# Kernel optimization log

Measured on AMD Instinct MI355X. Metric: run time of the kernel, lower is better.

## Reference

```python
import jax, jax.numpy as jnp
import numpy as np

MAX_DEPTH = 12  # 2^12-1 = 4095 internal nodes, 4096 leaves
NUM_INPUT = 1024
NUM_OUTPUT = 1024
BATCH = 4096


def setup_inputs() -> dict:
    key = jax.random.key(0)
    k1, k2, k3 = jax.random.split(key, 3)
    n_internal = (1 << MAX_DEPTH) - 1
    n_leaves = 1 << MAX_DEPTH
    x = jax.random.normal(k1, (BATCH, NUM_INPUT), dtype=jnp.float32)
    # per-node weights ~ N(0, 0.1) as in nn.Parameter(torch.empty(num_input).normal_(0, 0.1))
    W = jax.random.normal(k2, (n_internal, NUM_INPUT), dtype=jnp.float32) * 0.1
    b = jnp.zeros((n_internal,), dtype=jnp.float32)
    # leaf prob_dist initialized to ones in the original
    leaf = jnp.ones((n_leaves, NUM_OUTPUT), dtype=jnp.float32)
    # use random leaves so the blend is non-trivial for correctness checking
    leaf = leaf + jax.random.normal(k3, (n_leaves, NUM_OUTPUT), dtype=jnp.float32)
    return {"x": x, "W": W, "b": b, "leaf": leaf}


def reference(x, W, b, leaf):
    # W rows are internal nodes in level order: [root | level1 (2) | level2 (4) | ...]
    # Gate value at each node: sigmoid(x . w + b); output blends right with weight g,
    # left with weight (1-g), recursively -> leaf mixture weights are products of
    # gate / (1-gate) along each root-to-leaf path.
    B = x.shape[0]
    g = jax.nn.sigmoid(jnp.einsum('bi,ni->bn', x, W) + b)  # [B, n_internal]
    probs = jnp.ones((B, 1), dtype=x.dtype)
    idx = 0
    for d in range(MAX_DEPTH):  # structural loop over tree levels (fixed, small)
        n = 1 << d
        gl = g[:, idx:idx + n]  # gates at level d, [B, n]
        idx += n
        # children interleaved: [L0, R0, L1, R1, ...]; left weight (1-g), right g
        probs = jnp.stack([probs * (1.0 - gl), probs * gl], axis=-1).reshape(B, 2 * n)
    # output = sum over leaves of path_prob * leaf_dist
    out = jnp.einsum('bl,lo->bo', probs, leaf)  # [B, num_output]
    return out
```

## Files before the change

### kernel.cpp

```cpp
#include <hip/hip_runtime.h>
#include <hip/hip_bf16.h>
#include <hip/hip_fp16.h>

typedef _Float16 half8 __attribute__((ext_vector_type(8)));
typedef _Float16 half4 __attribute__((ext_vector_type(4)));
typedef float floatx4 __attribute__((ext_vector_type(4)));

#define BATCH   4096
#define NIN     1024
#define NODES   4095
#define NPAD    4096
#define NOUT    1024
#define NLEAF   4096
#define SPLITK  4

__device__ __forceinline__ void gload_lds16(const void* g, void* l) {
    __builtin_amdgcn_global_load_lds(
        (const __attribute__((address_space(1))) void*)g,
        (__attribute__((address_space(3))) void*)l, 16, 0, 0);
}

#define BAR() asm volatile("s_barrier" ::: "memory")

__global__ void k_f32_to_f16_pad(const float* __restrict__ src,
                                 _Float16* __restrict__ dst, int n, int nsrc) {
    int i = (blockIdx.x * blockDim.x + threadIdx.x) * 4;
    if (i >= n) return;
    float4 v;
    if (i < nsrc) v = *(const float4*)(src + i);
    else          v = make_float4(0.f, 0.f, 0.f, 0.f);
    half4 h;
    h.x = (_Float16)v.x; h.y = (_Float16)v.y;
    h.z = (_Float16)v.z; h.w = (_Float16)v.w;
    *(half4*)(dst + i) = h;
}

__global__ void k_transpose_f16(const float* __restrict__ src,
                                _Float16* __restrict__ dst) {
    __shared__ _Float16 t[32][33];
    int l0 = blockIdx.x * 32, o0 = blockIdx.y * 32;
    int tx = threadIdx.x & 31, ty = threadIdx.x >> 5;
#pragma unroll
    for (int i = 0; i < 4; i++) {
        int l = l0 + ty + i * 8;
        t[ty + i * 8][tx] = (_Float16)src[(size_t)l * NOUT + o0 + tx];
    }
    __syncthreads();
#pragma unroll
    for (int i = 0; i < 4; i++) {
        int o = o0 + ty + i * 8;
        dst[(size_t)o * NLEAF + l0 + tx] = t[tx][ty + i * 8];
    }
}

#define MFMA_CL(QR, QC, BARR, KK)                                               \
  _Pragma("unroll") for (int fr = 0; fr < 4; fr++)                              \
    _Pragma("unroll") for (int fc = 0; fc < 2; fc++)                            \
      acc[QR][QC][fr][fc] = __builtin_amdgcn_mfma_f32_16x16x32_f16(             \
          af[fr][KK], BARR[fc][KK], acc[QR][QC][fr][fc], 0, 0, 0);

template <int EPILOGUE>
__launch_bounds__(512, 2)
__global__ void gemm256(const _Float16* __restrict__ A,
                        const _Float16* __restrict__ Bm,
                        const float* __restrict__ bias,
                        void* __restrict__ C,
                        int M, int N, int K, int ldc, int Klen) {
    __shared__ __align__(16) _Float16 As[2][2][128 * 64];
    __shared__ __align__(16) _Float16 Bs[2][2][128 * 64];
    const int tid  = threadIdx.x;
    const int lane = tid & 63;
    const int wid  = tid >> 6;
    const int wm   = wid >> 2;
    const int wn   = wid & 3;
    const int m0 = blockIdx.y * 256;
    const int n0 = blockIdx.x * 256;
    const int k0 = blockIdx.z * Klen;
    (void)N;

    floatx4 acc[2][2][4][2] = {};
    half8 af[4][2];
    half8 bf0[2][2];
    half8 bf1[2][2];

    const int r1 = tid >> 3;
    const int c1 = (tid & 7) ^ (r1 & 7);
    const _Float16* Abase = A  + (size_t)(m0 + r1) * K + k0 + c1 * 8;
    const _Float16* Bbase = Bm + (size_t)(n0 + r1) * K + k0 + c1 * 8;

    auto stageA = [&](int bufx, int h, int T) {
        const _Float16* s = Abase + (size_t)h * 128 * K + T * 64;
        gload_lds16(s,                    &As[bufx][h][tid * 8]);
        gload_lds16(s + (size_t)64 * K,   &As[bufx][h][4096 + tid * 8]);
    };
    auto stageB = [&](int bufx, int h, int T) {
        const _Float16* s = Bbase + (size_t)h * 128 * K + T * 64;
        gload_lds16(s,                    &Bs[bufx][h][tid * 8]);
        gload_lds16(s + (size_t)64 * K,   &Bs[bufx][h][4096 + tid * 8]);
    };

    const int l4   = lane >> 4;
    const int arow = wm * 64 + (lane & 15);
    const int brow = wn * 32 + (lane & 15);
    const int pA0 = ((l4)     ^ (arow & 7)) * 8;
    const int pA1 = ((4 + l4) ^ (arow & 7)) * 8;
    const int pB0 = ((l4)     ^ (brow & 7)) * 8;
    const int pB1 = ((4 + l4) ^ (brow & 7)) * 8;

    const int NTt = Klen >> 6;

    stageA(0, 0, 0); stageB(0, 0, 0); stageA(0, 1, 0); stageB(0, 1, 0);
    if (NTt > 1) {
        stageA(1, 0, 1); stageB(1, 1, 1);
        asm volatile("s_waitcnt vmcnt(4)" ::: "memory");
    } else {
        asm volatile("s_waitcnt vmcnt(0)" ::: "memory");
    }
    BAR();

    for (int T = 0; T < NTt; ++T) {
        const int buf = T & 1;
        const _Float16* A0 = &As[buf][0][0];
        const _Float16* A1 = &As[buf][1][0];
        const _Float16* B0 = &Bs[buf][0][0];
        const _Float16* B1 = &Bs[buf][1][0];

#pragma unroll
        for (int fr = 0; fr < 4; fr++) {
            af[fr][0] = *(const half8*)(A0 + (arow + fr * 16) * 64 + pA0);
            af[fr][1] = *(const half8*)(A0 + (arow + fr * 16) * 64 + pA1);
        }
#pragma unroll
        for (int fc = 0; fc < 2; fc++) {
            bf0[fc][0] = *(const half8*)(B0 + (brow + fc * 16) * 64 + pB0);
            bf0[fc][1] = *(const half8*)(B0 + (brow + fc * 16) * 64 + pB1);
        }
        if (T + 1 < NTt) stageA(buf ^ 1, 1, T + 1);
        __builtin_amdgcn_s_setprio(1);
        MFMA_CL(0, 0, bf0, 0);
        MFMA_CL(0, 0, bf0, 1);
        __builtin_amdgcn_s_setprio(0);
        BAR();

#pragma unroll
        for (int fc = 0; fc < 2; fc++) {
            bf1[fc][0] = *(const half8*)(B1 + (brow + fc * 16) * 64 + pB0);
            bf1[fc][1] = *(const half8*)(B1 + (brow + fc * 16) * 64 + pB1);
        }
        if (T + 1 < NTt) stageB(buf ^ 1, 0, T + 1);
        __builtin_amdgcn_s_setprio(1);
        MFMA_CL(0, 1, bf1, 0);
        MFMA_CL(0, 1, bf1, 1);
        __builtin_amdgcn_s_setprio(0);
        BAR();

#pragma unroll
        for (int fr = 0; fr < 4; fr++) {
            af[fr][0] = *(const half8*)(A1 + (arow + fr * 16) * 64 + pA0);
            af[fr][1] = *(const half8*)(A1 + (arow + fr * 16) * 64 + pA1);
        }
        if (T + 2 < NTt) stageA(buf, 0, T + 2);
        __builtin_amdgcn_s_setprio(1);
        MFMA_CL(1, 1, bf1, 0);
        MFMA_CL(1, 1, bf1, 1);
        __builtin_amdgcn_s_setprio(0);
        BAR();

        if (T + 2 < NTt) stageB(buf, 1, T + 2);
        __builtin_amdgcn_s_setprio(1);
        MFMA_CL(1, 0, bf0, 0);
        MFMA_CL(1, 0, bf0, 1);
        __builtin_amdgcn_s_setprio(0);
        if (T + 1 < NTt) {
            if (T + 2 < NTt) asm volatile("s_waitcnt vmcnt(4)" ::: "memory");
            else             asm volatile("s_waitcnt vmcnt(0)" ::: "memory");
        }
        BAR();
    }

    const int erow = m0 + wm * 64 + l4 * 4;
    const int ecol = n0 + wn * 32 + (lane & 15);
    _Float16* Cp = (_Float16*)C + (EPILOGUE == 2 ? (size_t)blockIdx.z * M * ldc : 0);
#pragma unroll
    for (int qr = 0; qr < 2; qr++)
#pragma unroll
        for (int qc = 0; qc < 2; qc++)
#pragma unroll
            for (int fr = 0; fr < 4; fr++)
#pragma unroll
                for (int fc = 0; fc < 2; fc++) {
                    const int col = ecol + qc * 128 + fc * 16;
#pragma unroll
                    for (int rj = 0; rj < 4; rj++) {
                        const int row = erow + qr * 128 + fr * 16 + rj;
                        float v = acc[qr][qc][fr][fc][rj];
                        if (EPILOGUE == 1) {
                            float bb = (col < NODES) ? bias[col] : 0.f;
                            float z = v + bb;
                            Cp[(size_t)row * ldc + col] =
                                (_Float16)(1.f / (1.f + __expf(-z)));
                        } else {
                            Cp[(size_t)row * ldc + col] = (_Float16)v;
                        }
                    }
                }
}

__global__ void k_reduce4(const _Float16* __restrict__ part, float* __restrict__ out) {
    const size_t S = (size_t)BATCH * NOUT;
    size_t i = ((size_t)blockIdx.x * 256 + threadIdx.x) * 8;
    half8 a = *(const half8*)(part + i);
    half8 b = *(const half8*)(part + S + i);
    half8 c = *(const half8*)(part + 2 * S + i);
    half8 d = *(const half8*)(part + 3 * S + i);
    float4 lo, hi;
    lo.x = (float)a[0] + (float)b[0] + (float)c[0] + (float)d[0];
    lo.y = (float)a[1] + (float)b[1] + (float)c[1] + (float)d[1];
    lo.z = (float)a[2] + (float)b[2] + (float)c[2] + (float)d[2];
    lo.w = (float)a[3] + (float)b[3] + (float)c[3] + (float)d[3];
    hi.x = (float)a[4] + (float)b[4] + (float)c[4] + (float)d[4];
    hi.y = (float)a[5] + (float)b[5] + (float)c[5] + (float)d[5];
    hi.z = (float)a[6] + (float)b[6] + (float)c[6] + (float)d[6];
    hi.w = (float)a[7] + (float)b[7] + (float)c[7] + (float)d[7];
    *(float4*)(out + i) = lo;
    *(float4*)(out + i + 4) = hi;
}

__global__ void k_probs(const _Float16* __restrict__ g,
                        _Float16* __restrict__ probs) {
    __shared__ float gs[NPAD];
    const int b = blockIdx.x;
    const _Float16* grow = g + (size_t)b * NPAD;
#pragma unroll
    for (int it = 0; it < 2; it++) {
        int i = threadIdx.x + it * 256;
        half8 v = *(const half8*)(grow + i * 8);
#pragma unroll
        for (int j = 0; j < 8; j++) gs[i * 8 + j] = (float)v[j];
    }
    __syncthreads();
    const int t = threadIdx.x;
    float p = 1.f;
#pragma unroll
    for (int d = 0; d < 8; d++) {
        int node = (1 << d) - 1 + (t >> (8 - d));
        float gg = gs[node];
        int bit = (t >> (7 - d)) & 1;
        p *= bit ? gg : (1.f - gg);
    }
    float p9[2], p10[4], p11[8], p12[16];
    {
        float gg = gs[255 + t];
        p9[0] = p * (1.f - gg); p9[1] = p * gg;
    }
#pragma unroll
    for (int i = 0; i < 2; i++) {
        float gg = gs[511 + 2 * t + i];
        p10[2 * i] = p9[i] * (1.f - gg); p10[2 * i + 1] = p9[i] * gg;
    }
#pragma unroll
    for (int i = 0; i < 4; i++) {
        float gg = gs[1023 + 4 * t + i];
        p11[2 * i] = p10[i] * (1.f - gg); p11[2 * i + 1] = p10[i] * gg;
    }
#pragma unroll
    for (int i = 0; i < 8; i++) {
        float gg = gs[2047 + 8 * t + i];
        p12[2 * i] = p11[i] * (1.f - gg); p12[2 * i + 1] = p11[i] * gg;
    }
    half8 o0, o1;
#pragma unroll
    for (int j = 0; j < 8; j++) { o0[j] = (_Float16)p12[j]; o1[j] = (_Float16)p12[8 + j]; }
    _Float16* pr = probs + (size_t)b * NLEAF + t * 16;
    *(half8*)(pr) = o0;
    *(half8*)(pr + 8) = o1;
}

extern "C" void kernel_launch(void* const* d_in, const int* in_sizes, int n_in,
                              void* d_out, int out_size, void* d_ws, size_t ws_size,
                              hipStream_t stream) {
    (void)in_sizes; (void)n_in; (void)out_size; (void)ws_size;
    const float* x    = (const float*)d_in[0];
    const float* W    = (const float*)d_in[1];
    const float* bias = (const float*)d_in[2];
    const float* leaf = (const float*)d_in[3];
    float* out = (float*)d_out;

    _Float16* base  = (_Float16*)d_ws;
    _Float16* leafT = base;
    _Float16* probs = base + (size_t)4 * 1024 * 1024;
    _Float16* xh    = base + (size_t)20 * 1024 * 1024;
    _Float16* Wh    = base + (size_t)24 * 1024 * 1024;
    _Float16* g     = base + (size_t)28 * 1024 * 1024;
    _Float16* part  = xh;

    k_f32_to_f16_pad<<<(BATCH * NIN / 4 + 255) / 256, 256, 0, stream>>>(
        x, xh, BATCH * NIN, BATCH * NIN);
    k_f32_to_f16_pad<<<(NPAD * NIN / 4 + 255) / 256, 256, 0, stream>>>(
        W, Wh, NPAD * NIN, NODES * NIN);
    k_transpose_f16<<<dim3(NLEAF / 32, NOUT / 32), 256, 0, stream>>>(leaf, leafT);

    gemm256<1><<<dim3(NPAD / 256, BATCH / 256, 1), 512, 0, stream>>>(
        xh, Wh, bias, (void*)g, BATCH, NPAD, NIN, NPAD, NIN);

    k_probs<<<BATCH, 256, 0, stream>>>(g, probs);

    gemm256<2><<<dim3(NOUT / 256, BATCH / 256, SPLITK), 512, 0, stream>>>(
        probs, leafT, nullptr, (void*)part, BATCH, NOUT, NLEAF, NOUT, NLEAF / SPLITK);

    k_reduce4<<<(BATCH * NOUT) / (256 * 8), 256, 0, stream>>>(part, out);
}
```

Baseline: 133.2 us.

## Restructure GEMM main loop to prefetch next-tile LDS fragments across phases

Reorders the four-phase MFMA loop so the A and B fragments for the next K tile are read from LDS during the current tile's later phases. Separate register sets (af0/af1, bf0c/bf0n) are double-buffered, and the global-to-LDS staging order and waitcnt placement change to match. The goal is to hide LDS read latency behind MFMA work at the start of each tile. The cost is higher register pressure under launch_bounds(512,2), which could cause spills or lower occupancy, plus subtler hazards around the vmcnt/barrier ordering.

Result: slower. 174.7 us (+31.2%).

```diff
diff --git a/kernel.cpp b/kernel.cpp
--- a/kernel.cpp
+++ b/kernel.cpp
@@ -53,11 +53,11 @@
     }
 }
 
-#define MFMA_CL(QR, QC, BARR, KK)                                               \
+#define MFMA_CL(QR, QC, AARR, BARRV, KK)                                        \
   _Pragma("unroll") for (int fr = 0; fr < 4; fr++)                              \
     _Pragma("unroll") for (int fc = 0; fc < 2; fc++)                            \
       acc[QR][QC][fr][fc] = __builtin_amdgcn_mfma_f32_16x16x32_f16(             \
-          af[fr][KK], BARR[fc][KK], acc[QR][QC][fr][fc], 0, 0, 0);
+          AARR[fr][KK], BARRV[fc][KK], acc[QR][QC][fr][fc], 0, 0, 0);
 
 template <int EPILOGUE>
 __launch_bounds__(512, 2)
@@ -79,8 +79,10 @@
     (void)N;
 
     floatx4 acc[2][2][4][2] = {};
-    half8 af[4][2];
-    half8 bf0[2][2];
+    half8 af0[4][2];
+    half8 af1[4][2];
+    half8 bf0c[2][2];
+    half8 bf0n[2][2];
     half8 bf1[2][2];
 
     const int r1 = tid >> 3;
@@ -109,73 +111,97 @@
 
     const int NTt = Klen >> 6;
 
-    stageA(0, 0, 0); stageB(0, 0, 0); stageA(0, 1, 0); stageB(0, 1, 0);
+    stageB(0, 0, 0); stageA(0, 0, 0); stageB(0, 1, 0); stageA(0, 1, 0);
     if (NTt > 1) {
-        stageA(1, 0, 1); stageB(1, 1, 1);
-        asm volatile("s_waitcnt vmcnt(4)" ::: "memory");
+        stageB(1, 0, 1); stageA(1, 0, 1); stageB(1, 1, 1);
+        asm volatile("s_waitcnt vmcnt(6)" ::: "memory");
     } else {
         asm volatile("s_waitcnt vmcnt(0)" ::: "memory");
     }
     BAR();
+#pragma unroll
+    for (int fr = 0; fr < 4; fr++) {
+        af0[fr][0] = *(const half8*)(&As[0][0][(arow + fr * 16) * 64 + pA0]);
+        af0[fr][1] = *(const half8*)(&As[0][0][(arow + fr * 16) * 64 + pA1]);
+    }
+#pragma unroll
+    for (int fc = 0; fc < 2; fc++) {
+        bf0c[fc][0] = *(const half8*)(&Bs[0][0][(brow + fc * 16) * 64 + pB0]);
+        bf0c[fc][1] = *(const half8*)(&Bs[0][0][(brow + fc * 16) * 64 + pB1]);
+    }
 
     for (int T = 0; T < NTt; ++T) {
         const int buf = T & 1;
-        const _Float16* A0 = &As[buf][0][0];
-        const _Float16* A1 = &As[buf][1][0];
-        const _Float16* B0 = &Bs[buf][0][0];
-        const _Float16* B1 = &Bs[buf][1][0];
-
-#pragma unroll
-        for (int fr = 0; fr < 4; fr++) {
-            af[fr][0] = *(const half8*)(A0 + (arow + fr * 16) * 64 + pA0);
-            af[fr][1] = *(const half8*)(A0 + (arow + fr * 16) * 64 + pA1);
-        }
+        const _Float16* A_c = &As[buf][0][0];
+        const _Float16* B_c = &Bs[buf][0][0];
+        const _Float16* A_n = &As[buf ^ 1][0][0];
+        const _Float16* B_n = &Bs[buf ^ 1][0][0];
+
 #pragma unroll
         for (int fc = 0; fc < 2; fc++) {
-            bf0[fc][0] = *(const half8*)(B0 + (brow + fc * 16) * 64 + pB0);
-            bf0[fc][1] = *(const half8*)(B0 + (brow + fc * 16) * 64 + pB1);
+            bf1[fc][0] = *(const half8*)(B_c + 8192 + (brow + fc * 16) * 64 + pB0);
+            bf1[fc][1] = *(const half8*)(B_c + 8192 + (brow + fc * 16) * 64 + pB1);
         }
         if (T + 1 < NTt) stageA(buf ^ 1, 1, T + 1);
         __builtin_amdgcn_s_setprio(1);
-        MFMA_CL(0, 0, bf0, 0);
-        MFMA_CL(0, 0, bf0, 1);
-        __builtin_amdgcn_s_setprio(0);
-        BAR();
-
-#pragma unroll
-        for (int fc = 0; fc < 2; fc++) {
-            bf1[fc][0] = *(const half8*)(B1 + (brow + fc * 16) * 64 + pB0);
-            bf1[fc][1] = *(const half8*)(B1 + (brow + fc * 16) * 64 + pB1);
-        }
-        if (T + 1 < NTt) stageB(buf ^ 1, 0, T + 1);
-        __builtin_amdgcn_s_setprio(1);
-        MFMA_CL(0, 1, bf1, 0);
-        MFMA_CL(0, 1, bf1, 1);
-        __builtin_amdgcn_s_setprio(0);
-        BAR();
-
-#pragma unroll
-        for (int fr = 0; fr < 4; fr++) {
-            af[fr][0] = *(const half8*)(A1 + (arow + fr * 16) * 64 + pA0);
-            af[fr][1] = *(const half8*)(A1 + (arow + fr * 16) * 64 + pA1);
-        }
-        if (T + 2 < NTt) stageA(buf, 0, T + 2);
-        __builtin_amdgcn_s_setprio(1);
-        MFMA_CL(1, 1, bf1, 0);
-        MFMA_CL(1, 1, bf1, 1);
-        __builtin_amdgcn_s_setprio(0);
-        BAR();
-
-        if (T + 2 < NTt) stageB(buf, 1, T + 2);
-        __builtin_amdgcn_s_setprio(1);
-        MFMA_CL(1, 0, bf0, 0);
-        MFMA_CL(1, 0, bf0, 1);
+        MFMA_CL(0, 0, af0, bf0c, 0);
+        MFMA_CL(0, 0, af0, bf0c, 1);
         __builtin_amdgcn_s_setprio(0);
         if (T + 1 < NTt) {
             if (T + 2 < NTt) asm volatile("s_waitcnt vmcnt(4)" ::: "memory");
             else             asm volatile("s_waitcnt vmcnt(0)" ::: "memory");
         }
         BAR();
+
+#pragma unroll
+        for (int fr = 0; fr < 4; fr++) {
+            af1[fr][0] = *(const half8*)(A_c + 8192 + (arow + fr * 16) * 64 + pA0);
+            af1[fr][1] = *(const half8*)(A_c + 8192 + (arow + fr * 16) * 64 + pA1);
+        }
+        if (T + 2 < NTt) stageB(buf, 0, T + 2);
+        __builtin_amdgcn_s_setprio(1);
+        MFMA_CL(0, 1, af0, bf1, 0);
+        MFMA_CL(0, 1, af0, bf1, 1);
+        __builtin_amdgcn_s_setprio(0);
+        BAR();
+
+        if (T + 1 < NTt) {
+#pragma unroll
+            for (int fc = 0; fc < 2; fc++) {
+                bf0n[fc][0] = *(const half8*)(B_n + (brow + fc * 16) * 64 + pB0);
+                bf0n[fc][1] = *(const half8*)(B_n + (brow + fc * 16) * 64 + pB1);
+            }
+        }
+        if (T + 2 < NTt) stageA(buf, 0, T + 2);
+        __builtin_amdgcn_s_setprio(1);
+        MFMA_CL(1, 1, af1, bf1, 0);
+        MFMA_CL(1, 1, af1, bf1, 1);
+        __builtin_amdgcn_s_setprio(0);
+        if (T + 1 < NTt) {
+            if (T + 2 < NTt) asm volatile("s_waitcnt vmcnt(4)" ::: "memory");
+            else             asm volatile("s_waitcnt vmcnt(0)" ::: "memory");
+        }
+        BAR();
+
+        if (T + 1 < NTt) {
+#pragma unroll
+            for (int fr = 0; fr < 4; fr++) {
+                af0[fr][0] = *(const half8*)(A_n + (arow + fr * 16) * 64 + pA0);
+                af0[fr][1] = *(const half8*)(A_n + (arow + fr * 16) * 64 + pA1);
+            }
+        }
+        if (T + 2 < NTt) stageB(buf, 1, T + 2);
+        __builtin_amdgcn_s_setprio(1);
+        MFMA_CL(1, 0, af1, bf0c, 0);
+        MFMA_CL(1, 0, af1, bf0c, 1);
+        __builtin_amdgcn_s_setprio(0);
+        BAR();
+
+#pragma unroll
+        for (int fc = 0; fc < 2; fc++) {
+            bf0c[fc][0] = bf0n[fc][0];
+            bf0c[fc][1] = bf0n[fc][1];
+        }
     }
 
     const int erow = m0 + wm * 64 + l4 * 4;
```
